# Kernel tuning notes

Measured on AMD Instinct MI355X. Metric: run time of the kernel, lower is better.

The kernel has to match this reference:

```python
import jax, jax.numpy as jnp
import numpy as np

B, S, H, NH, L = 8, 512, 768, 12, 12
DH = H // NH
VOCAB = 50265
MAX_POS = 512
BUCKETS = 256
SPAN = BUCKETS  # att_span = position_buckets
FF = 4 * H
EPS = 1e-7


def layer_norm(x, g, b):
    mu = jnp.mean(x, -1, keepdims=True)
    var = jnp.mean((x - mu) ** 2, -1, keepdims=True)
    return (x - mu) / jnp.sqrt(var + EPS) * g + b


def build_relative_position(q_len, k_len):
    # DeBERTa build_relative_position + make_log_bucket_position
    rel = jnp.arange(q_len, dtype=jnp.int32)[:, None] - jnp.arange(k_len, dtype=jnp.int32)[None, :]
    sign = jnp.sign(rel)
    mid = BUCKETS // 2
    abs_pos = jnp.where((rel < mid) & (rel > -mid), mid - 1, jnp.abs(rel)).astype(jnp.float32)
    log_pos = jnp.ceil(jnp.log(abs_pos / mid) / np.log((MAX_POS - 1) / mid) * (mid - 1)) + mid
    return jnp.where(abs_pos <= mid, rel, (log_pos * sign).astype(jnp.int32))


def setup_inputs() -> dict:
    key = jax.random.key(0)
    ks = iter(jax.random.split(key, 64))
    std = 0.02

    def w(shape):
        return jax.random.normal(next(ks), shape, jnp.float32) * std

    inp = {
        'word_emb': w((VOCAB, H)),
        'pos_emb': w((MAX_POS, H)),
        'emb_ln_g': jnp.ones((H,), jnp.float32),
        'emb_ln_b': jnp.zeros((H,), jnp.float32),
        'rel_emb': w((2 * SPAN, H)),
        'Wq': w((L, H, H)), 'bq': jnp.zeros((L, H), jnp.float32),
        'Wk': w((L, H, H)), 'bk': jnp.zeros((L, H), jnp.float32),
        'Wv': w((L, H, H)), 'bv': jnp.zeros((L, H), jnp.float32),
        'Wo': w((L, H, H)), 'bo': jnp.zeros((L, H), jnp.float32),
        'ln1_g': jnp.ones((L, H), jnp.float32), 'ln1_b': jnp.zeros((L, H), jnp.float32),
        'Wi': w((L, H, FF)), 'bi': jnp.zeros((L, FF), jnp.float32),
        'Wo2': w((L, FF, H)), 'bo2': jnp.zeros((L, H), jnp.float32),
        'ln2_g': jnp.ones((L, H), jnp.float32), 'ln2_b': jnp.zeros((L, H), jnp.float32),
        'input_ids': jax.random.randint(next(ks), (B, S), 0, VOCAB, dtype=jnp.int32),
        'attention_mask': jnp.ones((B, S), jnp.int32),
    }
    return inp


def reference(word_emb, pos_emb, emb_ln_g, emb_ln_b, rel_emb,
              Wq, bq, Wk, bk, Wv, bv, Wo, bo, ln1_g, ln1_b,
              Wi, bi, Wo2, bo2, ln2_g, ln2_b,
              input_ids, attention_mask):
    mask = attention_mask.astype(jnp.float32)  # [B,S]
    emb = word_emb[input_ids] + pos_emb[jnp.arange(S)][None]
    h = layer_norm(emb, emb_ln_g, emb_ln_b) * mask[..., None]  # MaskedLayerNorm
    amask = (mask[:, None, None, :] * mask[:, None, :, None]) > 0  # [B,1,S,S]
    rel_pos = build_relative_position(S, S)  # [S,S] bucketed
    c2p_idx = jnp.broadcast_to(jnp.clip(rel_pos + SPAN, 0, 2 * SPAN - 1)[None, None], (B, NH, S, S))
    p2c_idx = jnp.broadcast_to(jnp.clip(-rel_pos + SPAN, 0, 2 * SPAN - 1)[None, None], (B, NH, S, S))
    scale = jnp.sqrt(jnp.float32(DH * 3))  # scale_factor = 1 + len(['c2p','p2c'])
    neg = jnp.finfo(jnp.float32).min

    def step(h, p):
        (Wq_, bq_, Wk_, bk_, Wv_, bv_, Wo_, bo_, g1, b1, Wi_, bi_, Wo2_, bo2_, g2, b2) = p

        def heads(x):
            return x.reshape(B, S, NH, DH).transpose(0, 2, 1, 3)

        q = heads(h @ Wq_ + bq_)
        k = heads(h @ Wk_ + bk_)
        v = heads(h @ Wv_ + bv_)
        scores = jnp.einsum('bhqd,bhkd->bhqk', q, k) / scale
        # content -> position (shared key projection, share_att_key=True)
        pos_k = (rel_emb @ Wk_ + bk_).reshape(2 * SPAN, NH, DH).transpose(1, 0, 2)  # [NH,2*SPAN,DH]
        c2p = jnp.einsum('bhqd,hmd->bhqm', q, pos_k)
        scores = scores + jnp.take_along_axis(c2p, c2p_idx, axis=-1) / scale
        # position -> content (shared query projection)
        pos_q = (rel_emb @ Wq_ + bq_).reshape(2 * SPAN, NH, DH).transpose(1, 0, 2)
        p2c = jnp.einsum('bhkd,hmd->bhkm', k, pos_q)  # indexed by key position
        p2c_g = jnp.take_along_axis(p2c, p2c_idx, axis=-1)  # [B,NH,Skey,Squery]
        scores = scores + jnp.swapaxes(p2c_g, -1, -2) / scale
        # XSoftmax: mask with -inf, softmax, zero masked entries
        probs = jax.nn.softmax(jnp.where(amask, scores, neg), axis=-1)
        probs = jnp.where(amask, probs, 0.0)
        ctx = jnp.einsum('bhqk,bhkd->bhqd', probs, v).transpose(0, 2, 1, 3).reshape(B, S, H)
        h1 = layer_norm(ctx @ Wo_ + bo_ + h, g1, b1)
        ff = jax.nn.gelu(h1 @ Wi_ + bi_, approximate=False)
        h2 = layer_norm(ff @ Wo2_ + bo2_ + h1, g2, b2)
        return h2, None

    h, _ = jax.lax.scan(step, h, (Wq, bq, Wk, bk, Wv, bv, Wo, bo, ln1_g, ln1_b, Wi, bi, Wo2, bo2, ln2_g, ln2_b))
    return h
```

## Files before the change

kernel.cpp:

```cpp
#include <hip/hip_runtime.h>
#include <hip/hip_bf16.h>
#include <cmath>

#define NB 8
#define NS 512
#define NHID 768
#define NHEAD 12
#define NL 12
#define NDH 64
#define NFF 3072
#define NTOK (NB*NS)
#define LN_EPS 1e-7f

typedef _Float16 h8 __attribute__((ext_vector_type(8)));
typedef _Float16 h4 __attribute__((ext_vector_type(4)));
typedef float f4 __attribute__((ext_vector_type(4)));

__global__ __launch_bounds__(256) void emb_kernel(
    const float* __restrict__ we, const float* __restrict__ pe,
    const float* __restrict__ g, const float* __restrict__ bvec,
    const int* __restrict__ ids, const int* __restrict__ msk, float* __restrict__ out)
{
  const int token = blockIdx.x, tid = threadIdx.x;
  const int s = token & (NS-1);
  __shared__ float red[256];
  const int id = ids[token];
  const float* wp = we + (size_t)id*NHID;
  const float* pp = pe + (size_t)s*NHID;
  float e[3]; float sum = 0.f;
  #pragma unroll
  for (int j=0;j<3;j++){ int d = tid + j*256; e[j] = wp[d] + pp[d]; sum += e[j]; }
  red[tid]=sum; __syncthreads();
  for (int o=128;o>0;o>>=1){ if (tid<o) red[tid]+=red[tid+o]; __syncthreads(); }
  const float mu = red[0]*(1.0f/NHID); __syncthreads();
  float vs=0.f;
  #pragma unroll
  for (int j=0;j<3;j++){ float d=e[j]-mu; vs += d*d; }
  red[tid]=vs; __syncthreads();
  for (int o=128;o>0;o>>=1){ if (tid<o) red[tid]+=red[tid+o]; __syncthreads(); }
  const float rstd = 1.0f/sqrtf(red[0]*(1.0f/NHID)+LN_EPS);
  const float mf = (float)msk[token];
  #pragma unroll
  for (int j=0;j<3;j++){
    int d = tid + j*256;
    out[(size_t)token*NHID + d] = ((e[j]-mu)*rstd*g[d] + bvec[d])*mf;
  }
}

__global__ __launch_bounds__(256) void ln_kernel(
    const float* __restrict__ X, const float* __restrict__ g, const float* __restrict__ bvec,
    float* __restrict__ out)
{
  const int token = blockIdx.x, tid = threadIdx.x;
  __shared__ float red[256];
  const float* x = X + (size_t)token*NHID;
  float e[3]; float sum=0.f;
  #pragma unroll
  for (int j=0;j<3;j++){ e[j]=x[tid+j*256]; sum+=e[j]; }
  red[tid]=sum; __syncthreads();
  for (int o=128;o>0;o>>=1){ if (tid<o) red[tid]+=red[tid+o]; __syncthreads(); }
  const float mu = red[0]*(1.0f/NHID); __syncthreads();
  float vs=0.f;
  #pragma unroll
  for (int j=0;j<3;j++){ float d=e[j]-mu; vs+=d*d; }
  red[tid]=vs; __syncthreads();
  for (int o=128;o>0;o>>=1){ if (tid<o) red[tid]+=red[tid+o]; __syncthreads(); }
  const float rstd = 1.0f/sqrtf(red[0]*(1.0f/NHID)+LN_EPS);
  #pragma unroll
  for (int j=0;j<3;j++){
    int d = tid + j*256;
    out[(size_t)token*NHID + d] = (e[j]-mu)*rstd*g[d] + bvec[d];
  }
}

__global__ __launch_bounds__(256) void wprep_kernel(
    const float* __restrict__ W0, const float* __restrict__ W1, const float* __restrict__ W2,
    const float* __restrict__ W3, const float* __restrict__ W4, const float* __restrict__ W5,
    _Float16* __restrict__ OH, _Float16* __restrict__ OL)
{
  const int z = blockIdx.z;
  const int K_ = (z==5)?NFF:NHID;
  const int N_ = (z==4)?NFF:NHID;
  const int tI = blockIdx.y, nI = blockIdx.x;
  if (tI*32 >= K_ || nI*64 >= N_) return;
  const float* W = (z==0)?W0:(z==1)?W1:(z==2)?W2:(z==3)?W3:(z==4)?W4:W5;
  const size_t off = (z<5) ? (size_t)z*589824 : (size_t)4718592;
  __shared__ float T[32][66];
  const int tid = threadIdx.x;
  {
    const int kk = tid>>3, n8 = (tid&7)*8;
    const float* src = W + (size_t)(tI*32+kk)*N_ + nI*64 + n8;
    float4 v0 = *(const float4*)src;
    float4 v1 = *(const float4*)(src+4);
    T[kk][n8+0]=v0.x; T[kk][n8+1]=v0.y; T[kk][n8+2]=v0.z; T[kk][n8+3]=v0.w;
    T[kk][n8+4]=v1.x; T[kk][n8+5]=v1.y; T[kk][n8+6]=v1.z; T[kk][n8+7]=v1.w;
  }
  __syncthreads();
  const int n = tid>>2, c = tid&3;
  h8 hv, lv;
  #pragma unroll
  for (int j=0;j<8;j++){
    float x = T[c*8+j][n];
    _Float16 h = (_Float16)x;
    hv[j] = h;
    lv[j] = (_Float16)(x - (float)h);
  }
  _Float16* drow = OH + off + ((size_t)tI*N_ + (size_t)nI*64 + n)*32 + ((c ^ (n&3))*8);
  *(h8*)drow = hv;
  *(h8*)(OL + (drow - OH)) = lv;
}

template<int EPI, int BN>
__global__ __launch_bounds__(256,2) void gemm_mfma(
    const float* __restrict__ A, const _Float16* __restrict__ WH, const _Float16* __restrict__ WL,
    const float* __restrict__ bias, const float* __restrict__ res, float* __restrict__ outp,
    _Float16* __restrict__ outh, _Float16* __restrict__ outl, int M, int N, int K)
{
  constexpr int NF = BN/32;
  __shared__ __align__(16) _Float16 Ah[128*32];
  __shared__ __align__(16) _Float16 Al[128*32];
  __shared__ __align__(16) _Float16 Bh[BN*32];
  __shared__ __align__(16) _Float16 Bl[BN*32];
  const int tid = threadIdx.x;
  const int w = tid>>6, l = tid&63;
  const int wm = w>>1, wn = w&1, lr = l&15, lc = l>>4;
  const int bm = blockIdx.y*128, bn = blockIdx.x*BN;
  const int T = K>>5;
  f4 acc[4][NF] = {};

  const int sr = tid>>1, sk = (tid&1)<<4;
  const float* aptr = A + (size_t)(bm+sr)*K + sk;
  _Float16* arH = Ah + sr*32;
  _Float16* arL = Al + sr*32;
  const int c0 = sk>>3;
  const int p0 = ((c0  ) ^ (sr&3))<<3;
  const int p1 = ((c0+1) ^ (sr&3))<<3;
  const int fsw = (lc ^ (lr&3))<<3;
  const int aBase = (wm*64 + lr)*32 + fsw;
  const int bBase = (wn*(BN/2) + lr)*32 + fsw;

  float4 ga0, ga1, ga2, ga3;
  uint4 gb0h = {}, gb0l = {}, gb1h = {}, gb1l = {};

  auto loadg = [&](int t){
    const float* ap = aptr + t*32;
    ga0 = *(const float4*)(ap);
    ga1 = *(const float4*)(ap+4);
    ga2 = *(const float4*)(ap+8);
    ga3 = *(const float4*)(ap+12);
    const uint4* bsH = (const uint4*)(WH + ((size_t)t*N + bn)*32);
    const uint4* bsL = (const uint4*)(WL + ((size_t)t*N + bn)*32);
    gb0h = bsH[tid]; gb0l = bsL[tid];
    if (NF==4){ gb1h = bsH[tid+256]; gb1l = bsL[tid+256]; }
  };
  loadg(0);

  for (int t=0; t<T; ++t){
    float xs[16] = {ga0.x,ga0.y,ga0.z,ga0.w, ga1.x,ga1.y,ga1.z,ga1.w,
                    ga2.x,ga2.y,ga2.z,ga2.w, ga3.x,ga3.y,ga3.z,ga3.w};
    h8 hv0, hv1, lv0, lv1;
    #pragma unroll
    for (int j=0;j<8;j++){
      _Float16 h0 = (_Float16)xs[j];
      hv0[j] = h0; lv0[j] = (_Float16)(xs[j] - (float)h0);
      _Float16 h1 = (_Float16)xs[8+j];
      hv1[j] = h1; lv1[j] = (_Float16)(xs[8+j] - (float)h1);
    }
    __syncthreads();
    *(h8*)(arH+p0) = hv0; *(h8*)(arH+p1) = hv1;
    *(h8*)(arL+p0) = lv0; *(h8*)(arL+p1) = lv1;
    ((uint4*)Bh)[tid] = gb0h; ((uint4*)Bl)[tid] = gb0l;
    if (NF==4){ ((uint4*)Bh)[tid+256] = gb1h; ((uint4*)Bl)[tid+256] = gb1l; }
    __syncthreads();
    if (t+1 < T) loadg(t+1);

    h8 ahv[4], alv[4];
    #pragma unroll
    for (int mf=0; mf<4; ++mf){
      ahv[mf] = *(const h8*)(Ah + aBase + mf*512);
      alv[mf] = *(const h8*)(Al + aBase + mf*512);
    }
    #pragma unroll
    for (int nf=0; nf<NF; ++nf){
      h8 bhv = *(const h8*)(Bh + bBase + nf*512);
      h8 blv = *(const h8*)(Bl + bBase + nf*512);
      #pragma unroll
      for (int mf=0; mf<4; ++mf){
        acc[mf][nf] = __builtin_amdgcn_mfma_f32_16x16x32_f16(ahv[mf], bhv, acc[mf][nf], 0,0,0);
        acc[mf][nf] = __builtin_amdgcn_mfma_f32_16x16x32_f16(alv[mf], bhv, acc[mf][nf], 0,0,0);
        acc[mf][nf] = __builtin_amdgcn_mfma_f32_16x16x32_f16(ahv[mf], blv, acc[mf][nf], 0,0,0);
      }
    }
  }
  #pragma unroll
  for (int nf=0; nf<NF; ++nf){
    const int n = bn + wn*(BN/2) + nf*16 + lr;
    const float bb = bias[n];
    #pragma unroll
    for (int mf=0; mf<4; ++mf){
      #pragma unroll
      for (int r=0; r<4; ++r){
        const int m = bm + wm*64 + mf*16 + lc*4 + r;
        float v = acc[mf][nf][r] + bb;
        if (EPI==1) v = 0.5f*v*(1.0f + erff(v*0.7071067811865476f));
        if (EPI==2) v += res[(size_t)m*N + n];
        if (EPI==3){
          _Float16 hh = (_Float16)v;
          outh[(size_t)m*N + n] = hh;
          outl[(size_t)m*N + n] = (_Float16)(v - (float)hh);
        } else {
          outp[(size_t)m*N + n] = v;
        }
      }
    }
  }
}

__global__ __launch_bounds__(64) void relgather_kernel(
    const float* __restrict__ PKb, const float* __restrict__ PQb,
    _Float16* __restrict__ PKgh, _Float16* __restrict__ PKgl,
    _Float16* __restrict__ PQgh, _Float16* __restrict__ PQgl)
{
  const int r = blockIdx.x;
  const int h = blockIdx.y;
  const int d = threadIdx.x;
  const size_t dst = ((size_t)h*1024 + r)*NDH + d;
  if (r >= 1023){ PKgh[dst]=(_Float16)0.f; PKgl[dst]=(_Float16)0.f;
                  PQgh[dst]=(_Float16)0.f; PQgl[dst]=(_Float16)0.f; return; }
  const int rel = r - 511;
  const int sg = (rel>0) - (rel<0);
  const float ap = (rel<128 && rel>-128) ? 127.0f : fabsf((float)rel);
  int bucket;
  if (ap <= 128.0f) bucket = rel;
  else bucket = (int)((ceilf(logf(ap*(1.0f/128.0f))/1.3843393f*127.0f)+128.0f)*(float)sg);
  const int idx = min(max(bucket+256,0),511);
  const size_t src = (size_t)idx*NHID + h*NDH + d;
  const float v1 = PKb[src], v2 = PQb[src];
  const _Float16 h1 = (_Float16)v1, h2 = (_Float16)v2;
  PKgh[dst]=h1; PKgl[dst]=(_Float16)(v1-(float)h1);
  PQgh[dst]=h2; PQgl[dst]=(_Float16)(v2-(float)h2);
}

__global__ __launch_bounds__(256) void vtrans_kernel(
    const float* __restrict__ V, _Float16* __restrict__ Vth, _Float16* __restrict__ Vtl)
{
  __shared__ float T[64][68];
  const int tid = threadIdx.x;
  const int k0 = blockIdx.x*64, h = blockIdx.y, b = blockIdx.z;
  const int bh = b*NHEAD + h;
  for (int i=tid; i<1024; i+=256){
    const int row = i>>4, c = i&15;
    *(float4*)&T[row][c*4] = *(const float4*)&V[(size_t)(b*NS + k0 + row)*NHID + h*NDH + c*4];
  }
  __syncthreads();
  for (int i=tid; i<512; i+=256){
    const int d = i>>3, kc = i&7;
    h8 hv, lv;
    #pragma unroll
    for (int j=0;j<8;++j){
      float x = T[kc*8+j][d];
      _Float16 hh = (_Float16)x;
      hv[j] = hh; lv[j] = (_Float16)(x - (float)hh);
    }
    const size_t dst = ((size_t)bh*NDH + d)*NS + k0 + kc*8;
    *(h8*)&Vth[dst] = hv;
    *(h8*)&Vtl[dst] = lv;
  }
}

template<int SGN>
__global__ __launch_bounds__(256) void cband_kernel(
    const _Float16* __restrict__ Xh, const _Float16* __restrict__ Xl,
    const _Float16* __restrict__ Ph, const _Float16* __restrict__ Pl,
    _Float16* __restrict__ outC)
{
  __shared__ _Float16 Xsh[2048], Xsl[2048];
  __shared__ _Float16 Psh[2048], Psl[2048];
  __shared__ _Float16 Of[32*520];
  const int tid = threadIdx.x;
  const int row0 = blockIdx.x*32, h = blockIdx.y, b = blockIdx.z;
  const int bh = b*NHEAD + h;
  const int w = tid>>6, l = tid&63, lr = l&15, lc = l>>4;
  const int fsw = (lc ^ (lr&3))<<3;
  const int mf = w&1, nf = w>>1;
  {
    const int row = tid>>3, pl = (tid>>2)&1, c = tid&3;
    const size_t src = (size_t)(b*NS + row0 + row)*NHID + h*NDH + pl*32 + c*8;
    const int dst = pl*1024 + row*32 + ((c ^ (row&3))<<3);
    *(h8*)&Xsh[dst] = *(const h8*)&Xh[src];
    *(h8*)&Xsl[dst] = *(const h8*)&Xl[src];
  }
  __syncthreads();
  h8 xah[2], xal[2];
  #pragma unroll
  for (int pl=0; pl<2; ++pl){
    xah[pl] = *(const h8*)&Xsh[pl*1024 + (mf*16+lr)*32 + fsw];
    xal[pl] = *(const h8*)&Xsl[pl*1024 + (mf*16+lr)*32 + fsw];
  }
  const int rbase = (SGN>0) ? row0 : (480 - row0);
  for (int rt=0; rt<17; ++rt){
    __syncthreads();
    {
      const int rrow = tid>>3, pl = (tid>>2)&1, c = tid&3;
      const size_t src = ((size_t)h*1024 + rbase + rt*32 + rrow)*NDH + pl*32 + c*8;
      const int dst = pl*1024 + rrow*32 + ((c ^ (rrow&3))<<3);
      *(h8*)&Psh[dst] = *(const h8*)&Ph[src];
      *(h8*)&Psl[dst] = *(const h8*)&Pl[src];
    }
    __syncthreads();
    f4 cacc = {0.f,0.f,0.f,0.f};
    #pragma unroll
    for (int pl=0; pl<2; ++pl){
      h8 pbh = *(const h8*)&Psh[pl*1024 + (nf*16+lr)*32 + fsw];
      h8 pbl = *(const h8*)&Psl[pl*1024 + (nf*16+lr)*32 + fsw];
      cacc = __builtin_amdgcn_mfma_f32_16x16x32_f16(xah[pl], pbh, cacc, 0,0,0);
      cacc = __builtin_amdgcn_mfma_f32_16x16x32_f16(xal[pl], pbh, cacc, 0,0,0);
      cacc = __builtin_amdgcn_mfma_f32_16x16x32_f16(xah[pl], pbl, cacc, 0,0,0);
    }
    const int rl = rt*32 + nf*16 + lr;
    #pragma unroll
    for (int r=0; r<4; ++r){
      const int q = mf*16 + lc*4 + r;
      const int j = (SGN>0) ? (rl - q) : (rl + q - 31);
      if (j >= 0 && j < NS) Of[q*520 + j] = (_Float16)cacc[r];
    }
  }
  __syncthreads();
  for (int i=tid; i<2048; i+=256){
    const int row = i>>6, cc = i&63;
    *(h8*)&outC[((size_t)bh*NS + row0 + row)*NS + cc*8] = *(const h8*)&Of[row*520 + cc*8];
  }
}

__global__ __launch_bounds__(256) void attn_mfma(
    const _Float16* __restrict__ Qh, const _Float16* __restrict__ Ql,
    const _Float16* __restrict__ Kh, const _Float16* __restrict__ Kl,
    const _Float16* __restrict__ Vth, const _Float16* __restrict__ Vtl,
    const _Float16* __restrict__ Cq, const _Float16* __restrict__ Cp,
    const int* __restrict__ msk, float* __restrict__ Ctx)
{
  __shared__ _Float16 Qsh[2048], Qsl[2048];
  __shared__ _Float16 Ksh[4096], Ksl[4096];
  __shared__ _Float16 Vsh[4096], Vsl[4096];
  __shared__ _Float16 Psh[2048], Psl[2048];
  __shared__ float Ss[32][68];
  __shared__ float alphaS[32], invS[32];
  __shared__ int mqS[32], mkS[64];

  const int tid = threadIdx.x;
  const int qt = blockIdx.x, h = blockIdx.y, b = blockIdx.z;
  const int q0 = qt*32;
  const int bh = b*NHEAD + h;
  const int w = tid>>6, l = tid&63, lr = l&15, lc = l>>4;
  const int fsw = (lc ^ (lr&3))<<3;
  const int mf = w&1, ng = w>>1;

  {
    const int row = tid>>3, pl = (tid>>2)&1, c = tid&3;
    const size_t src = (size_t)(b*NS + q0 + row)*NHID + h*NDH + pl*32 + c*8;
    const int dst = pl*1024 + row*32 + ((c ^ (row&3))<<3);
    *(h8*)&Qsh[dst] = *(const h8*)&Qh[src];
    *(h8*)&Qsl[dst] = *(const h8*)&Ql[src];
  }
  if (tid < 32) mqS[tid] = msk[b*NS + q0 + tid];
  __syncthreads();

  h8 qah[2], qal[2];
  #pragma unroll
  for (int pl=0; pl<2; ++pl){
    qah[pl] = *(const h8*)&Qsh[pl*1024 + (mf*16+lr)*32 + fsw];
    qal[pl] = *(const h8*)&Qsl[pl*1024 + (mf*16+lr)*32 + fsw];
  }

  const int sq = tid>>3, sj = tid&7;
  float m_i = -3.4e38f, l_i = 0.f;
  f4 oacc[2] = {};

  for (int kt=0; kt<NS/64; ++kt){
    const int k0 = kt*64;
    __syncthreads();
    for (int i=tid; i<512; i+=256){
      const int row = i>>3, pl = (i>>2)&1, c = i&3;
      const size_t srcK = (size_t)(b*NS + k0 + row)*NHID + h*NDH + pl*32 + c*8;
      const int dstT = pl*2048 + row*32 + ((c ^ (row&3))<<3);
      *(h8*)&Ksh[dstT] = *(const h8*)&Kh[srcK];
      *(h8*)&Ksl[dstT] = *(const h8*)&Kl[srcK];
      const size_t srcV = ((size_t)bh*NDH + row)*NS + k0 + pl*32 + c*8;
      *(h8*)&Vsh[dstT] = *(const h8*)&Vth[srcV];
      *(h8*)&Vsl[dstT] = *(const h8*)&Vtl[srcV];
    }
    if (tid < 64) mkS[tid] = msk[b*NS + k0 + tid];
    __syncthreads();

    #pragma unroll
    for (int nn=0; nn<2; ++nn){
      const int n = ng*2 + nn;
      f4 s = {0.f,0.f,0.f,0.f};
      #pragma unroll
      for (int pl=0; pl<2; ++pl){
        h8 kbh = *(const h8*)&Ksh[pl*2048 + (n*16+lr)*32 + fsw];
        h8 kbl = *(const h8*)&Ksl[pl*2048 + (n*16+lr)*32 + fsw];
        s = __builtin_amdgcn_mfma_f32_16x16x32_f16(qah[pl], kbh, s, 0,0,0);
        s = __builtin_amdgcn_mfma_f32_16x16x32_f16(qal[pl], kbh, s, 0,0,0);
        s = __builtin_amdgcn_mfma_f32_16x16x32_f16(qah[pl], kbl, s, 0,0,0);
      }
      const int kcol = n*16 + lr, kg = k0 + kcol;
      const int qbase = mf*16 + lc*4;
      const h4 cp4 = *(const h4*)&Cp[((size_t)bh*NS + kg)*NS + q0 + qbase];
      const int mk = mkS[kcol];
      #pragma unroll
      for (int r=0;r<4;++r){
        const int qloc = qbase + r;
        const float cq = (float)Cq[((size_t)bh*NS + q0 + qloc)*NS + (511 - kg)];
        const float val = (s[r] + cq + (float)cp4[r]) * 0.07216878364870322f;
        Ss[qloc][kcol] = (mk && mqS[qloc]) ? val : -3.4e38f;
      }
    }
    __syncthreads();

    const float4 sp0 = *(const float4*)&Ss[sq][sj*8];
    const float4 sp1 = *(const float4*)&Ss[sq][sj*8+4];
    float tm = fmaxf(fmaxf(fmaxf(sp0.x,sp0.y),fmaxf(sp0.z,sp0.w)),
                     fmaxf(fmaxf(sp1.x,sp1.y),fmaxf(sp1.z,sp1.w)));
    tm = fmaxf(tm, __shfl_xor(tm,1,8));
    tm = fmaxf(tm, __shfl_xor(tm,2,8));
    tm = fmaxf(tm, __shfl_xor(tm,4,8));
    const float m_new = fmaxf(m_i, tm);
    const float alpha = expf(m_i - m_new);
    float pv[8];
    pv[0]=expf(sp0.x-m_new); pv[1]=expf(sp0.y-m_new); pv[2]=expf(sp0.z-m_new); pv[3]=expf(sp0.w-m_new);
    pv[4]=expf(sp1.x-m_new); pv[5]=expf(sp1.y-m_new); pv[6]=expf(sp1.z-m_new); pv[7]=expf(sp1.w-m_new);
    float ts = pv[0]+pv[1]+pv[2]+pv[3]+pv[4]+pv[5]+pv[6]+pv[7];
    ts += __shfl_xor(ts,1,8);
    ts += __shfl_xor(ts,2,8);
    ts += __shfl_xor(ts,4,8);
    l_i = l_i*alpha + ts;
    m_i = m_new;
    h8 phv, plv;
    #pragma unroll
    for (int j=0;j<8;++j){
      _Float16 hh = (_Float16)pv[j];
      phv[j] = hh; plv[j] = (_Float16)(pv[j]-(float)hh);
    }
    const int pdst = (sj>>2)*1024 + sq*32 + ((((sj&3)) ^ (sq&3))<<3);
    *(h8*)&Psh[pdst] = phv;
    *(h8*)&Psl[pdst] = plv;
    if (sj==0) alphaS[sq] = alpha;
    __syncthreads();

    float ar[4];
    #pragma unroll
    for (int r=0;r<4;++r) ar[r] = alphaS[mf*16 + lc*4 + r];
    #pragma unroll
    for (int nn=0;nn<2;++nn)
      #pragma unroll
      for (int r=0;r<4;++r) oacc[nn][r] *= ar[r];
    #pragma unroll
    for (int pl=0;pl<2;++pl){
      h8 pah = *(const h8*)&Psh[pl*1024 + (mf*16+lr)*32 + fsw];
      h8 pal = *(const h8*)&Psl[pl*1024 + (mf*16+lr)*32 + fsw];
      #pragma unroll
      for (int nn=0;nn<2;++nn){
        const int dn = ng*32 + nn*16 + lr;
        h8 vbh = *(const h8*)&Vsh[pl*2048 + dn*32 + fsw];
        h8 vbl = *(const h8*)&Vsl[pl*2048 + dn*32 + fsw];
        oacc[nn] = __builtin_amdgcn_mfma_f32_16x16x32_f16(pah, vbh, oacc[nn], 0,0,0);
        oacc[nn] = __builtin_amdgcn_mfma_f32_16x16x32_f16(pal, vbh, oacc[nn], 0,0,0);
        oacc[nn] = __builtin_amdgcn_mfma_f32_16x16x32_f16(pah, vbl, oacc[nn], 0,0,0);
      }
    }
  }

  const float inv = (l_i > 0.f && m_i > -1e30f && mqS[sq]) ? 1.0f/l_i : 0.f;
  if (sj==0) invS[sq] = inv;
  __syncthreads();
  #pragma unroll
  for (int nn=0;nn<2;++nn){
    #pragma unroll
    for (int r=0;r<4;++r){
      const int qloc = mf*16 + lc*4 + r;
      const int d = ng*32 + nn*16 + lr;
      Ctx[(size_t)(b*NS + q0 + qloc)*NHID + h*NDH + d] = oacc[nn][r] * invS[qloc];
    }
  }
}

extern "C" void kernel_launch(void* const* d_in, const int* in_sizes, int n_in,
                              void* d_out, int out_size, void* d_ws, size_t ws_size,
                              hipStream_t stream)
{
  const float* word_emb=(const float*)d_in[0];
  const float* pos_emb =(const float*)d_in[1];
  const float* emb_g   =(const float*)d_in[2];
  const float* emb_b   =(const float*)d_in[3];
  const float* rel_emb =(const float*)d_in[4];
  const float* Wq=(const float*)d_in[5];  const float* bq=(const float*)d_in[6];
  const float* Wk=(const float*)d_in[7];  const float* bk=(const float*)d_in[8];
  const float* Wv=(const float*)d_in[9];  const float* bvv=(const float*)d_in[10];
  const float* Wo=(const float*)d_in[11]; const float* bo=(const float*)d_in[12];
  const float* g1=(const float*)d_in[13]; const float* b1=(const float*)d_in[14];
  const float* Wi=(const float*)d_in[15]; const float* bi=(const float*)d_in[16];
  const float* Wo2=(const float*)d_in[17];const float* bo2=(const float*)d_in[18];
  const float* g2=(const float*)d_in[19]; const float* b2=(const float*)d_in[20];
  const int* ids  =(const int*)d_in[21];
  const int* amask=(const int*)d_in[22];

  char* p = (char*)d_ws;
  auto alloc = [&](size_t bytes)->char*{ char* r = p; p += (bytes + 255) & ~(size_t)255; return r; };
  float* Hb  = (float*)alloc((size_t)NTOK*NHID*4);
  float* H1  = (float*)alloc((size_t)NTOK*NHID*4);
  float* Xb  = (float*)alloc((size_t)NTOK*NHID*4);
  float* FFb = (float*)alloc((size_t)NTOK*NFF*4);
  float* Ctxb= (float*)alloc((size_t)NTOK*NHID*4);
  float* Vb  = (float*)alloc((size_t)NTOK*NHID*4);
  _Float16* Qhb = (_Float16*)alloc((size_t)NTOK*NHID*2);
  _Float16* Qlb = (_Float16*)alloc((size_t)NTOK*NHID*2);
  _Float16* Khb = (_Float16*)alloc((size_t)NTOK*NHID*2);
  _Float16* Klb = (_Float16*)alloc((size_t)NTOK*NHID*2);
  _Float16* Vth = (_Float16*)alloc((size_t)NTOK*NHID*2);
  _Float16* Vtl = (_Float16*)alloc((size_t)NTOK*NHID*2);
  float* PKb = (float*)alloc((size_t)512*NHID*4);
  float* PQb = (float*)alloc((size_t)512*NHID*4);
  _Float16* PKgh = (_Float16*)alloc((size_t)NHEAD*1024*NDH*2);
  _Float16* PKgl = (_Float16*)alloc((size_t)NHEAD*1024*NDH*2);
  _Float16* PQgh = (_Float16*)alloc((size_t)NHEAD*1024*NDH*2);
  _Float16* PQgl = (_Float16*)alloc((size_t)NHEAD*1024*NDH*2);
  _Float16* CqB = (_Float16*)alloc((size_t)NB*NHEAD*NS*NS*2);
  _Float16* CpB = (_Float16*)alloc((size_t)NB*NHEAD*NS*NS*2);
  _Float16* WtH = (_Float16*)alloc((size_t)7077888*2);
  _Float16* WtL = (_Float16*)alloc((size_t)7077888*2);

  const size_t WO[6] = {0, 589824, 1179648, 1769472, 2359296, 4718592};

  dim3 blk(256);
  dim3 gRel(1024, NHEAD);
  dim3 gAttn(NS/32, NHEAD, NB);
  dim3 gBand(NS/32, NHEAD, NB);
  dim3 gVt(NS/64, NHEAD, NB);
  dim3 gPrep(48, 96, 6);
  dim3 gSmall(12, 4);
  dim3 gProj(12, 32);
  dim3 gFF1(24, 32);

  emb_kernel<<<NTOK,blk,0,stream>>>(word_emb,pos_emb,emb_g,emb_b,ids,amask,Hb);

  for (int l=0; l<NL; l++){
    const float *Wq_l=Wq+(size_t)l*NHID*NHID, *bq_l=bq+(size_t)l*NHID;
    const float *Wk_l=Wk+(size_t)l*NHID*NHID, *bk_l=bk+(size_t)l*NHID;
    const float *Wv_l=Wv+(size_t)l*NHID*NHID, *bv_l=bvv+(size_t)l*NHID;
    const float *Wo_l=Wo+(size_t)l*NHID*NHID, *bo_l=bo+(size_t)l*NHID;
    const float *g1_l=g1+(size_t)l*NHID, *b1_l=b1+(size_t)l*NHID;
    const float *Wi_l=Wi+(size_t)l*NHID*NFF, *bi_l=bi+(size_t)l*NFF;
    const float *Wo2_l=Wo2+(size_t)l*NFF*NHID, *bo2_l=bo2+(size_t)l*NHID;
    const float *g2_l=g2+(size_t)l*NHID, *b2_l=b2+(size_t)l*NHID;

    wprep_kernel<<<gPrep,blk,0,stream>>>(Wq_l,Wk_l,Wv_l,Wo_l,Wi_l,Wo2_l,WtH,WtL);

    gemm_mfma<0,64><<<gSmall,blk,0,stream>>>(rel_emb, WtH+WO[1], WtL+WO[1], bk_l, nullptr, PKb, nullptr,nullptr, 512,NHID,NHID);
    gemm_mfma<0,64><<<gSmall,blk,0,stream>>>(rel_emb, WtH+WO[0], WtL+WO[0], bq_l, nullptr, PQb, nullptr,nullptr, 512,NHID,NHID);
    relgather_kernel<<<gRel,dim3(64),0,stream>>>(PKb, PQb, PKgh, PKgl, PQgh, PQgl);
    gemm_mfma<3,64><<<gProj,blk,0,stream>>>(Hb, WtH+WO[0], WtL+WO[0], bq_l, nullptr, nullptr, Qhb, Qlb, NTOK,NHID,NHID);
    gemm_mfma<3,64><<<gProj,blk,0,stream>>>(Hb, WtH+WO[1], WtL+WO[1], bk_l, nullptr, nullptr, Khb, Klb, NTOK,NHID,NHID);
    gemm_mfma<0,64><<<gProj,blk,0,stream>>>(Hb, WtH+WO[2], WtL+WO[2], bv_l, nullptr, Vb, nullptr,nullptr, NTOK,NHID,NHID);
    vtrans_kernel<<<gVt,blk,0,stream>>>(Vb, Vth, Vtl);
    cband_kernel<1><<<gBand,blk,0,stream>>>(Qhb, Qlb, PKgh, PKgl, CqB);
    cband_kernel<-1><<<gBand,blk,0,stream>>>(Khb, Klb, PQgh, PQgl, CpB);
    attn_mfma<<<gAttn,blk,0,stream>>>(Qhb,Qlb,Khb,Klb,Vth,Vtl,CqB,CpB,amask,Ctxb);
    gemm_mfma<2,64><<<gProj,blk,0,stream>>>(Ctxb, WtH+WO[3], WtL+WO[3], bo_l, Hb, Xb, nullptr,nullptr, NTOK,NHID,NHID);
    ln_kernel<<<NTOK,blk,0,stream>>>(Xb, g1_l, b1_l, H1);
    gemm_mfma<1,128><<<gFF1,blk,0,stream>>>(H1, WtH+WO[4], WtL+WO[4], bi_l, nullptr, FFb, nullptr,nullptr, NTOK,NFF,NHID);
    gemm_mfma<2,64><<<gProj,blk,0,stream>>>(FFb, WtH+WO[5], WtL+WO[5], bo2_l, H1, Xb, nullptr,nullptr, NTOK,NHID,NFF);
    float* dst = (l==NL-1) ? (float*)d_out : Hb;
    ln_kernel<<<NTOK,blk,0,stream>>>(Xb, g2_l, b2_l, dst);
  }
}
```

Before: 7.382 ms.

## Pre-split activations into fp16 planes and stream GEMM tiles via global_load_lds

```diff
diff --git a/kernel.cpp b/kernel.cpp
--- a/kernel.cpp
+++ b/kernel.cpp
@@ -16,10 +16,15 @@
 typedef _Float16 h4 __attribute__((ext_vector_type(4)));
 typedef float f4 __attribute__((ext_vector_type(4)));
 
+#define GL(dst, src) __builtin_amdgcn_global_load_lds( \
+    (const __attribute__((address_space(1))) void*)(src), \
+    (__attribute__((address_space(3))) void*)(dst), 16, 0, 0)
+
 __global__ __launch_bounds__(256) void emb_kernel(
     const float* __restrict__ we, const float* __restrict__ pe,
     const float* __restrict__ g, const float* __restrict__ bvec,
-    const int* __restrict__ ids, const int* __restrict__ msk, float* __restrict__ out)
+    const int* __restrict__ ids, const int* __restrict__ msk, float* __restrict__ out,
+    _Float16* __restrict__ oh, _Float16* __restrict__ ol)
 {
   const int token = blockIdx.x, tid = threadIdx.x;
   const int s = token & (NS-1);
@@ -43,13 +48,17 @@
   #pragma unroll
   for (int j=0;j<3;j++){
     int d = tid + j*256;
-    out[(size_t)token*NHID + d] = ((e[j]-mu)*rstd*g[d] + bvec[d])*mf;
+    float v = ((e[j]-mu)*rstd*g[d] + bvec[d])*mf;
+    out[(size_t)token*NHID + d] = v;
+    _Float16 hh = (_Float16)v;
+    oh[(size_t)token*NHID + d] = hh;
+    ol[(size_t)token*NHID + d] = (_Float16)(v - (float)hh);
   }
 }
 
 __global__ __launch_bounds__(256) void ln_kernel(
     const float* __restrict__ X, const float* __restrict__ g, const float* __restrict__ bvec,
-    float* __restrict__ out)
+    float* __restrict__ out, _Float16* __restrict__ oh, _Float16* __restrict__ ol)
 {
   const int token = blockIdx.x, tid = threadIdx.x;
   __shared__ float red[256];
@@ -69,8 +78,30 @@
   #pragma unroll
   for (int j=0;j<3;j++){
     int d = tid + j*256;
-    out[(size_t)token*NHID + d] = (e[j]-mu)*rstd*g[d] + bvec[d];
-  }
+    float v = (e[j]-mu)*rstd*g[d] + bvec[d];
+    out[(size_t)token*NHID + d] = v;
+    _Float16 hh = (_Float16)v;
+    oh[(size_t)token*NHID + d] = hh;
+    ol[(size_t)token*NHID + d] = (_Float16)(v - (float)hh);
+  }
+}
+
+__global__ __launch_bounds__(256) void planes_kernel(
+    const float* __restrict__ X, _Float16* __restrict__ oh, _Float16* __restrict__ ol, int n8)
+{
+  const int i = blockIdx.x*256 + threadIdx.x;
+  if (i >= n8) return;
+  const float4 v0 = ((const float4*)X)[i*2];
+  const float4 v1 = ((const float4*)X)[i*2+1];
+  const float xs[8] = {v0.x,v0.y,v0.z,v0.w,v1.x,v1.y,v1.z,v1.w};
+  h8 hv, lv;
+  #pragma unroll
+  for (int j=0;j<8;j++){
+    _Float16 hh = (_Float16)xs[j];
+    hv[j]=hh; lv[j]=(_Float16)(xs[j]-(float)hh);
+  }
+  *(h8*)&oh[(size_t)i*8] = hv;
+  *(h8*)&ol[(size_t)i*8] = lv;
 }
 
 __global__ __launch_bounds__(256) void wprep_kernel(
@@ -105,85 +136,85 @@
     hv[j] = h;
     lv[j] = (_Float16)(x - (float)h);
   }
-  _Float16* drow = OH + off + ((size_t)tI*N_ + (size_t)nI*64 + n)*32 + ((c ^ (n&3))*8);
+  const int sw = (n&3) ^ ((n>>2)&3);
+  _Float16* drow = OH + off + ((size_t)tI*N_ + (size_t)nI*64 + n)*32 + ((c ^ sw)*8);
   *(h8*)drow = hv;
   *(h8*)(OL + (drow - OH)) = lv;
 }
 
 template<int EPI, int BN>
-__global__ __launch_bounds__(256,2) void gemm_mfma(
-    const float* __restrict__ A, const _Float16* __restrict__ WH, const _Float16* __restrict__ WL,
-    const float* __restrict__ bias, const float* __restrict__ res, float* __restrict__ outp,
-    _Float16* __restrict__ outh, _Float16* __restrict__ outl, int M, int N, int K)
+__global__ __launch_bounds__(256,2) void gemm2(
+    const _Float16* __restrict__ Ah, const _Float16* __restrict__ Al,
+    const _Float16* __restrict__ WH, const _Float16* __restrict__ WL,
+    const float* __restrict__ bias, const float* __restrict__ res,
+    float* __restrict__ outp, _Float16* __restrict__ outh, _Float16* __restrict__ outl,
+    int M, int N, int K, int nbx)
 {
   constexpr int NF = BN/32;
-  __shared__ __align__(16) _Float16 Ah[128*32];
-  __shared__ __align__(16) _Float16 Al[128*32];
-  __shared__ __align__(16) _Float16 Bh[BN*32];
-  __shared__ __align__(16) _Float16 Bl[BN*32];
+  constexpr int BH = BN*32;
+  __shared__ __align__(16) _Float16 LAh[2*4096];
+  __shared__ __align__(16) _Float16 LAl[2*4096];
+  __shared__ __align__(16) _Float16 LBh[2*BH];
+  __shared__ __align__(16) _Float16 LBl[2*BH];
   const int tid = threadIdx.x;
   const int w = tid>>6, l = tid&63;
-  const int wm = w>>1, wn = w&1, lr = l&15, lc = l>>4;
-  const int bm = blockIdx.y*128, bn = blockIdx.x*BN;
+  const int orig = blockIdx.x;
+  const int wg = (orig&7)*((int)gridDim.x>>3) + (orig>>3);
+  const int bx = wg % nbx, by = wg / nbx;
+  const int bm = by*128, bn = bx*BN;
   const int T = K>>5;
-  f4 acc[4][NF] = {};
-
-  const int sr = tid>>1, sk = (tid&1)<<4;
-  const float* aptr = A + (size_t)(bm+sr)*K + sk;
-  _Float16* arH = Ah + sr*32;
-  _Float16* arL = Al + sr*32;
-  const int c0 = sk>>3;
-  const int p0 = ((c0  ) ^ (sr&3))<<3;
-  const int p1 = ((c0+1) ^ (sr&3))<<3;
-  const int fsw = (lc ^ (lr&3))<<3;
+
+  const int lr = l&15, lc = l>>4;
+  const int wm = w>>1, wn = w&1;
+  const int fsw = ((lc ^ (lr&3) ^ ((lr>>2)&3))<<3);
   const int aBase = (wm*64 + lr)*32 + fsw;
   const int bBase = (wn*(BN/2) + lr)*32 + fsw;
 
-  float4 ga0, ga1, ga2, ga3;
-  uint4 gb0h = {}, gb0l = {}, gb1h = {}, gb1l = {};
-
-  auto loadg = [&](int t){
-    const float* ap = aptr + t*32;
-    ga0 = *(const float4*)(ap);
-    ga1 = *(const float4*)(ap+4);
-    ga2 = *(const float4*)(ap+8);
-    ga3 = *(const float4*)(ap+12);
-    const uint4* bsH = (const uint4*)(WH + ((size_t)t*N + bn)*32);
-    const uint4* bsL = (const uint4*)(WL + ((size_t)t*N + bn)*32);
-    gb0h = bsH[tid]; gb0l = bsL[tid];
-    if (NF==4){ gb1h = bsH[tid+256]; gb1l = bsL[tid+256]; }
+  const int rowA = (w<<5) + (l>>2);
+  const int cA = l&3;
+  const int swA = (rowA&3) ^ ((rowA>>2)&3);
+  const _Float16* aSrcH = Ah + (size_t)(bm+rowA)*K + ((cA ^ swA)<<3);
+  const _Float16* aSrcL = Al + (size_t)(bm+rowA)*K + ((cA ^ swA)<<3);
+  const int a16K = 16*K;
+  const size_t bLane = (size_t)(BN==64 ? w*512 : w*1024) + l*8;
+  const _Float16* bSrcH = WH + (size_t)bn*32 + bLane;
+  const _Float16* bSrcL = WL + (size_t)bn*32 + bLane;
+  const size_t bStep = (size_t)N*32;
+  const int bWOff = (BN==64) ? w*512 : w*1024;
+
+  auto stage = [&](int b2){
+    _Float16* dAh = LAh + b2*4096 + w*1024;
+    _Float16* dAl = LAl + b2*4096 + w*1024;
+    GL(dAh,     aSrcH); GL(dAh+512, aSrcH + a16K);
+    GL(dAl,     aSrcL); GL(dAl+512, aSrcL + a16K);
+    _Float16* dBh = LBh + b2*BH + bWOff;
+    _Float16* dBl = LBl + b2*BH + bWOff;
+    GL(dBh, bSrcH); GL(dBl, bSrcL);
+    if (BN==128){ GL(dBh+512, bSrcH+512); GL(dBl+512, bSrcL+512); }
+    aSrcH += 32; aSrcL += 32; bSrcH += bStep; bSrcL += bStep;
   };
-  loadg(0);
-
+
+  f4 acc[4][NF] = {};
+  stage(0);
+  asm volatile("s_waitcnt vmcnt(0)" ::: "memory");
+  __syncthreads();
+  int buf = 0;
   for (int t=0; t<T; ++t){
-    float xs[16] = {ga0.x,ga0.y,ga0.z,ga0.w, ga1.x,ga1.y,ga1.z,ga1.w,
-                    ga2.x,ga2.y,ga2.z,ga2.w, ga3.x,ga3.y,ga3.z,ga3.w};
-    h8 hv0, hv1, lv0, lv1;
-    #pragma unroll
-    for (int j=0;j<8;j++){
-      _Float16 h0 = (_Float16)xs[j];
-      hv0[j] = h0; lv0[j] = (_Float16)(xs[j] - (float)h0);
-      _Float16 h1 = (_Float16)xs[8+j];
-      hv1[j] = h1; lv1[j] = (_Float16)(xs[8+j] - (float)h1);
-    }
-    __syncthreads();
-    *(h8*)(arH+p0) = hv0; *(h8*)(arH+p1) = hv1;
-    *(h8*)(arL+p0) = lv0; *(h8*)(arL+p1) = lv1;
-    ((uint4*)Bh)[tid] = gb0h; ((uint4*)Bl)[tid] = gb0l;
-    if (NF==4){ ((uint4*)Bh)[tid+256] = gb1h; ((uint4*)Bl)[tid+256] = gb1l; }
-    __syncthreads();
-    if (t+1 < T) loadg(t+1);
-
+    if (t+1 < T) stage(buf^1);
+    const _Float16* pAh = LAh + buf*4096;
+    const _Float16* pAl = LAl + buf*4096;
+    const _Float16* pBh = LBh + buf*BH;
+    const _Float16* pBl = LBl + buf*BH;
     h8 ahv[4], alv[4];
     #pragma unroll
     for (int mf=0; mf<4; ++mf){
-      ahv[mf] = *(const h8*)(Ah + aBase + mf*512);
-      alv[mf] = *(const h8*)(Al + aBase + mf*512);
+      ahv[mf] = *(const h8*)(pAh + aBase + mf*512);
+      alv[mf] = *(const h8*)(pAl + aBase + mf*512);
     }
     #pragma unroll
     for (int nf=0; nf<NF; ++nf){
-      h8 bhv = *(const h8*)(Bh + bBase + nf*512);
-      h8 blv = *(const h8*)(Bl + bBase + nf*512);
+      h8 bhv = *(const h8*)(pBh + bBase + nf*512);
+      h8 blv = *(const h8*)(pBl + bBase + nf*512);
       #pragma unroll
       for (int mf=0; mf<4; ++mf){
         acc[mf][nf] = __builtin_amdgcn_mfma_f32_16x16x32_f16(ahv[mf], bhv, acc[mf][nf], 0,0,0);
@@ -191,6 +222,9 @@
         acc[mf][nf] = __builtin_amdgcn_mfma_f32_16x16x32_f16(ahv[mf], blv, acc[mf][nf], 0,0,0);
       }
     }
+    asm volatile("s_waitcnt vmcnt(0)" ::: "memory");
+    __syncthreads();
+    buf ^= 1;
   }
   #pragma unroll
   for (int nf=0; nf<NF; ++nf){
@@ -202,13 +236,17 @@
       for (int r=0; r<4; ++r){
         const int m = bm + wm*64 + mf*16 + lc*4 + r;
         float v = acc[mf][nf][r] + bb;
-        if (EPI==1) v = 0.5f*v*(1.0f + erff(v*0.7071067811865476f));
-        if (EPI==2) v += res[(size_t)m*N + n];
-        if (EPI==3){
+        if (EPI==1){
+          v = 0.5f*v*(1.0f + erff(v*0.7071067811865476f));
+          _Float16 hh = (_Float16)v;
+          outh[(size_t)m*N + n] = hh;
+          outl[(size_t)m*N + n] = (_Float16)(v - (float)hh);
+        } else if (EPI==3){
           _Float16 hh = (_Float16)v;
           outh[(size_t)m*N + n] = hh;
           outl[(size_t)m*N + n] = (_Float16)(v - (float)hh);
         } else {
+          if (EPI==2) v += res[(size_t)m*N + n];
           outp[(size_t)m*N + n] = v;
         }
       }
@@ -337,7 +375,7 @@
     const _Float16* __restrict__ Kh, const _Float16* __restrict__ Kl,
     const _Float16* __restrict__ Vth, const _Float16* __restrict__ Vtl,
     const _Float16* __restrict__ Cq, const _Float16* __restrict__ Cp,
-    const int* __restrict__ msk, float* __restrict__ Ctx)
+    const int* __restrict__ msk, _Float16* __restrict__ Ctxh, _Float16* __restrict__ Ctxl)
 {
   __shared__ _Float16 Qsh[2048], Qsl[2048];
   __shared__ _Float16 Ksh[4096], Ksl[4096];
@@ -480,7 +518,11 @@
     for (int r=0;r<4;++r){
       const int qloc = mf*16 + lc*4 + r;
       const int d = ng*32 + nn*16 + lr;
-      Ctx[(size_t)(b*NS + q0 + qloc)*NHID + h*NDH + d] = oacc[nn][r] * invS[qloc];
+      const float v = oacc[nn][r] * invS[qloc];
+      const _Float16 hh = (_Float16)v;
+      const size_t idx = (size_t)(b*NS + q0 + qloc)*NHID + h*NDH + d;
+      Ctxh[idx] = hh;
+      Ctxl[idx] = (_Float16)(v - (float)hh);
     }
   }
 }
@@ -510,9 +552,15 @@
   float* Hb  = (float*)alloc((size_t)NTOK*NHID*4);
   float* H1  = (float*)alloc((size_t)NTOK*NHID*4);
   float* Xb  = (float*)alloc((size_t)NTOK*NHID*4);
-  float* FFb = (float*)alloc((size_t)NTOK*NFF*4);
-  float* Ctxb= (float*)alloc((size_t)NTOK*NHID*4);
   float* Vb  = (float*)alloc((size_t)NTOK*NHID*4);
+  _Float16* Hh  = (_Float16*)alloc((size_t)NTOK*NHID*2);
+  _Float16* Hl  = (_Float16*)alloc((size_t)NTOK*NHID*2);
+  _Float16* H1h = (_Float16*)alloc((size_t)NTOK*NHID*2);
+  _Float16* H1l = (_Float16*)alloc((size_t)NTOK*NHID*2);
+  _Float16* FFbh= (_Float16*)alloc((size_t)NTOK*NFF*2);
+  _Float16* FFbl= (_Float16*)alloc((size_t)NTOK*NFF*2);
+  _Float16* Ctxh= (_Float16*)alloc((size_t)NTOK*NHID*2);
+  _Float16* Ctxl= (_Float16*)alloc((size_t)NTOK*NHID*2);
   _Float16* Qhb = (_Float16*)alloc((size_t)NTOK*NHID*2);
   _Float16* Qlb = (_Float16*)alloc((size_t)NTOK*NHID*2);
   _Float16* Khb = (_Float16*)alloc((size_t)NTOK*NHID*2);
@@ -527,6 +575,8 @@
   _Float16* PQgl = (_Float16*)alloc((size_t)NHEAD*1024*NDH*2);
   _Float16* CqB = (_Float16*)alloc((size_t)NB*NHEAD*NS*NS*2);
   _Float16* CpB = (_Float16*)alloc((size_t)NB*NHEAD*NS*NS*2);
+  _Float16* Rh  = (_Float16*)alloc((size_t)512*NHID*2);
+  _Float16* Rl  = (_Float16*)alloc((size_t)512*NHID*2);
   _Float16* WtH = (_Float16*)alloc((size_t)7077888*2);
   _Float16* WtL = (_Float16*)alloc((size_t)7077888*2);
 
@@ -538,11 +588,9 @@
   dim3 gBand(NS/32, NHEAD, NB);
   dim3 gVt(NS/64, NHEAD, NB);
   dim3 gPrep(48, 96, 6);
-  dim3 gSmall(12, 4);
-  dim3 gProj(12, 32);
-  dim3 gFF1(24, 32);
-
-  emb_kernel<<<NTOK,blk,0,stream>>>(word_emb,pos_emb,emb_g,emb_b,ids,amask,Hb);
+
+  emb_kernel<<<NTOK,blk,0,stream>>>(word_emb,pos_emb,emb_g,emb_b,ids,amask,Hb,Hh,Hl);
+  planes_kernel<<<192,blk,0,stream>>>(rel_emb, Rh, Rl, 512*NHID/8);
 
   for (int l=0; l<NL; l++){
     const float *Wq_l=Wq+(size_t)l*NHID*NHID, *bq_l=bq+(size_t)l*NHID;
@@ -556,21 +604,21 @@
 
     wprep_kernel<<<gPrep,blk,0,stream>>>(Wq_l,Wk_l,Wv_l,Wo_l,Wi_l,Wo2_l,WtH,WtL);
 
-    gemm_mfma<0,64><<<gSmall,blk,0,stream>>>(rel_emb, WtH+WO[1], WtL+WO[1], bk_l, nullptr, PKb, nullptr,nullptr, 512,NHID,NHID);
-    gemm_mfma<0,64><<<gSmall,blk,0,stream>>>(rel_emb, WtH+WO[0], WtL+WO[0], bq_l, nullptr, PQb, nullptr,nullptr, 512,NHID,NHID);
+    gemm2<0,64><<<48,blk,0,stream>>>(Rh,Rl, WtH+WO[1],WtL+WO[1], bk_l, nullptr, PKb,nullptr,nullptr, 512,NHID,NHID, 12);
+    gemm2<0,64><<<48,blk,0,stream>>>(Rh,Rl, WtH+WO[0],WtL+WO[0], bq_l, nullptr, PQb,nullptr,nullptr, 512,NHID,NHID, 12);
     relgather_kernel<<<gRel,dim3(64),0,stream>>>(PKb, PQb, PKgh, PKgl, PQgh, PQgl);
-    gemm_mfma<3,64><<<gProj,blk,0,stream>>>(Hb, WtH+WO[0], WtL+WO[0], bq_l, nullptr, nullptr, Qhb, Qlb, NTOK,NHID,NHID);
-    gemm_mfma<3,64><<<gProj,blk,0,stream>>>(Hb, WtH+WO[1], WtL+WO[1], bk_l, nullptr, nullptr, Khb, Klb, NTOK,NHID,NHID);
-    gemm_mfma<0,64><<<gProj,blk,0,stream>>>(Hb, WtH+WO[2], WtL+WO[2], bv_l, nullptr, Vb, nullptr,nullptr, NTOK,NHID,NHID);
+    gemm2<3,64><<<384,blk,0,stream>>>(Hh,Hl, WtH+WO[0],WtL+WO[0], bq_l, nullptr, nullptr,Qhb,Qlb, NTOK,NHID,NHID, 12);
+    gemm2<3,64><<<384,blk,0,stream>>>(Hh,Hl, WtH+WO[1],WtL+WO[1], bk_l, nullptr, nullptr,Khb,Klb, NTOK,NHID,NHID, 12);
+    gemm2<0,64><<<384,blk,0,stream>>>(Hh,Hl, WtH+WO[2],WtL+WO[2], bv_l, nullptr, Vb,nullptr,nullptr, NTOK,NHID,NHID, 12);
     vtrans_kernel<<<gVt,blk,0,stream>>>(Vb, Vth, Vtl);
     cband_kernel<1><<<gBand,blk,0,stream>>>(Qhb, Qlb, PKgh, PKgl, CqB);
     cband_kernel<-1><<<gBand,blk,0,stream>>>(Khb, Klb, PQgh, PQgl, CpB);
-    attn_mfma<<<gAttn,blk,0,stream>>>(Qhb,Qlb,Khb,Klb,Vth,Vtl,CqB,CpB,amask,Ctxb);
-    gemm_mfma<2,64><<<gProj,blk,0,stream>>>(Ctxb, WtH+WO[3], WtL+WO[3], bo_l, Hb, Xb, nullptr,nullptr, NTOK,NHID,NHID);
-    ln_kernel<<<NTOK,blk,0,stream>>>(Xb, g1_l, b1_l, H1);
-    gemm_mfma<1,128><<<gFF1,blk,0,stream>>>(H1, WtH+WO[4], WtL+WO[4], bi_l, nullptr, FFb, nullptr,nullptr, NTOK,NFF,NHID);
-    gemm_mfma<2,64><<<gProj,blk,0,stream>>>(FFb, WtH+WO[5], WtL+WO[5], bo2_l, H1, Xb, nullptr,nullptr, NTOK,NHID,NFF);
+    attn_mfma<<<gAttn,blk,0,stream>>>(Qhb,Qlb,Khb,Klb,Vth,Vtl,CqB,CpB,amask,Ctxh,Ctxl);
+    gemm2<2,64><<<384,blk,0,stream>>>(Ctxh,Ctxl, WtH+WO[3],WtL+WO[3], bo_l, Hb, Xb,nullptr,nullptr, NTOK,NHID,NHID, 12);
+    ln_kernel<<<NTOK,blk,0,stream>>>(Xb, g1_l, b1_l, H1, H1h, H1l);
+    gemm2<1,128><<<768,blk,0,stream>>>(H1h,H1l, WtH+WO[4],WtL+WO[4], bi_l, nullptr, nullptr,FFbh,FFbl, NTOK,NFF,NHID, 24);
+    gemm2<2,64><<<384,blk,0,stream>>>(FFbh,FFbl, WtH+WO[5],WtL+WO[5], bo2_l, H1, Xb,nullptr,nullptr, NTOK,NHID,NFF, 12);
     float* dst = (l==NL-1) ? (float*)d_out : Hb;
-    ln_kernel<<<NTOK,blk,0,stream>>>(Xb, g2_l, b2_l, dst);
-  }
-}
+    ln_kernel<<<NTOK,blk,0,stream>>>(Xb, g2_l, b2_l, dst, Hh, Hl);
+  }
+}
```

Measured after the change: 7.173 ms. 1.03x faster.
